# Optimization experiments

Measured on AMD Instinct MI355X. Metric: run time of the kernel, lower is better.

## Reference

```python
import jax, jax.numpy as jnp
import numpy as np

N_NODES = 50000
N_EDGES = 800000
IN_DIM = 256
HID = 64


def _gcn_conv(x, src, dst, W, b, num_nodes):
    # PyG GCNConv: h = D^{-1/2} (A + I) D^{-1/2} (x @ W) + b
    h = x @ W  # [N, out]
    loop = jnp.arange(num_nodes)
    s = jnp.concatenate([src, loop])  # add self-loops
    d = jnp.concatenate([dst, loop])
    deg = jax.ops.segment_sum(jnp.ones_like(s, dtype=h.dtype), d, num_segments=num_nodes)
    dinv = jnp.where(deg > 0, deg ** -0.5, 0.0)
    norm = dinv[s] * dinv[d]  # [E+N]
    msgs = h[s] * norm[:, None]  # gather + scale
    out = jax.ops.segment_sum(msgs, d, num_segments=num_nodes)  # scatter-add to dst
    return out + b


def setup_inputs() -> dict:
    key = jax.random.key(0)
    ks = jax.random.split(key, 8)
    x = jax.random.normal(ks[0], (N_NODES, IN_DIM), dtype=jnp.float32)
    edge_index = jax.random.randint(ks[1], (2, N_EDGES), 0, N_NODES, dtype=jnp.int64)
    # Glorot-ish init for weights
    W1 = jax.random.normal(ks[2], (IN_DIM, HID), dtype=jnp.float32) * (1.0 / np.sqrt(IN_DIM))
    b1 = jnp.zeros((HID,), dtype=jnp.float32)
    W2 = jax.random.normal(ks[3], (HID, HID), dtype=jnp.float32) * (1.0 / np.sqrt(HID))
    b2 = jnp.zeros((HID,), dtype=jnp.float32)
    Wc = jax.random.normal(ks[4], (HID, 1), dtype=jnp.float32) * (1.0 / np.sqrt(HID))
    bc = jnp.zeros((1,), dtype=jnp.float32)
    return {"x": x, "edge_index": edge_index, "W1": W1, "b1": b1, "W2": W2, "b2": b2, "Wc": Wc, "bc": bc}


def reference(x, edge_index, W1, b1, W2, b2, Wc, bc):
    num_nodes = x.shape[0]
    src, dst = edge_index[0], edge_index[1]
    h = jax.nn.relu(_gcn_conv(x, src, dst, W1, b1, num_nodes))
    h = jax.nn.relu(_gcn_conv(h, src, dst, W2, b2, num_nodes))
    return jax.nn.sigmoid(h @ Wc + bc)  # [N, 1]
```

## Files before the change

kernel.cpp:

```cpp
#include <hip/hip_runtime.h>
#include <math.h>

#define N_NODES 50000
#define N_EDGES 800000
#define IN_DIM 256
#define HID 64
#define BKT 256
#define NBKT ((N_NODES + BKT - 1) / BKT)
#define CAP 8192
#define CHUNK 4096
#define NCH ((N_EDGES + CHUNK - 1) / CHUNK)
#define NGB ((N_NODES + 63) / 64)

typedef short short8v __attribute__((ext_vector_type(8)));
typedef float f32x4 __attribute__((ext_vector_type(4)));
typedef unsigned uint4v __attribute__((ext_vector_type(4)));

__device__ __forceinline__ unsigned short f2bf(float f) {
  unsigned u = __builtin_bit_cast(unsigned, f);
  u += 0x7FFFu + ((u >> 16) & 1u);
  return (unsigned short)(u >> 16);
}
__device__ __forceinline__ unsigned pack2(float a, float b) {
  return (unsigned)f2bf(a) | ((unsigned)f2bf(b) << 16);
}
__device__ __forceinline__ float bfu_lo(unsigned u) {
  return __builtin_bit_cast(float, u << 16);
}
__device__ __forceinline__ float bfu_hi(unsigned u) {
  return __builtin_bit_cast(float, u & 0xFFFF0000u);
}

__global__ void k_prep(int* __restrict__ bcur, const float* __restrict__ W1,
                       const float* __restrict__ W2, unsigned short* __restrict__ Wt1,
                       unsigned short* __restrict__ Wt2) {
  const int t = threadIdx.x;
  if (blockIdx.x == 0) {
    bcur[t] = 0;
  } else if (blockIdx.x == 1) {
    for (int j = 0; j < 64; ++j) {
      int lin = j * 256 + t;
      int k = lin >> 6, c = lin & 63;
      Wt1[c * 256 + k] = f2bf(W1[lin]);
    }
  } else {
    for (int j = 0; j < 16; ++j) {
      int lin = j * 256 + t;
      int k = lin >> 6, c = lin & 63;
      Wt2[c * 64 + k] = f2bf(W2[lin]);
    }
  }
}

__global__ __launch_bounds__(256) void k_g1split(
    const float* __restrict__ X, const unsigned short* __restrict__ Wt1g,
    unsigned short* __restrict__ outA, const int* __restrict__ src,
    const int* __restrict__ dst, int* __restrict__ bcur, unsigned* __restrict__ ebuf) {
  __shared__ unsigned short Wl[64][IN_DIM + 8];
  __shared__ int cnt[NBKT];
  __shared__ int cur[NBKT];
  const int t = threadIdx.x;
  if (blockIdx.x < NGB) {
    const int lane = t & 63, wv = t >> 6;
#pragma unroll
    for (int j = 0; j < 8; ++j) {
      int grp = j * 256 + t;
      int r = grp >> 5, c = (grp & 31) * 8;
      *reinterpret_cast<short8v*>(&Wl[r][c]) =
          *reinterpret_cast<const short8v*>(&Wt1g[r * IN_DIM + c]);
    }
    const int row0 = blockIdx.x * 64;
    int r = row0 + wv * 16 + (lane & 15);
    if (r > N_NODES - 1) r = N_NODES - 1;
    const int kh = (lane >> 4) * 8;

    uint4v ap[8];
#pragma unroll
    for (int k0 = 0; k0 < 8; ++k0) {
      const float* Xp = X + (size_t)r * IN_DIM + k0 * 32 + kh;
      const float4 x0 = *reinterpret_cast<const float4*>(Xp);
      const float4 x1 = *reinterpret_cast<const float4*>(Xp + 4);
      uint4v p;
      p.x = pack2(x0.x, x0.y); p.y = pack2(x0.z, x0.w);
      p.z = pack2(x1.x, x1.y); p.w = pack2(x1.z, x1.w);
      ap[k0] = p;
    }
    __syncthreads();

    f32x4 acc[4] = {};
#pragma unroll
    for (int k0 = 0; k0 < 8; ++k0) {
      short8v a = __builtin_bit_cast(short8v, ap[k0]);
#pragma unroll
      for (int n = 0; n < 4; ++n) {
        short8v b = *reinterpret_cast<const short8v*>(&Wl[n * 16 + (lane & 15)][k0 * 32 + kh]);
        acc[n] = __builtin_amdgcn_mfma_f32_16x16x32_bf16(a, b, acc[n], 0, 0, 0);
      }
    }

    const int r0 = row0 + wv * 16;
#pragma unroll
    for (int j = 0; j < 4; ++j) {
      int rr = r0 + (lane >> 4) * 4 + j;
      if (rr < N_NODES) {
#pragma unroll
        for (int n = 0; n < 4; ++n)
          outA[(size_t)rr * 64 + n * 16 + (lane & 15)] = f2bf(acc[n][j]);
      }
    }
  } else {
    for (int i = t; i < NBKT; i += 256) cnt[i] = 0;
    __syncthreads();
    const int base = (blockIdx.x - NGB) * CHUNK;
#pragma unroll
    for (int i = 0; i < CHUNK / 256; ++i) {
      int e = base + i * 256 + t;
      if (e < N_EDGES) atomicAdd(&cnt[dst[e] >> 8], 1);
    }
    __syncthreads();
    for (int i = t; i < NBKT; i += 256) {
      int c = cnt[i];
      cur[i] = c ? (i * CAP + atomicAdd(&bcur[i], c)) : 0;
    }
    __syncthreads();
#pragma unroll
    for (int i = 0; i < CHUNK / 256; ++i) {
      int e = base + i * 256 + t;
      if (e < N_EDGES) {
        int d = dst[e];
        int p = atomicAdd(&cur[d >> 8], 1);
        ebuf[p] = ((unsigned)src[e] << 8) | (unsigned)(d & 255);
      }
    }
  }
}

__global__ void k_bucket(const unsigned* __restrict__ ebuf, const int* __restrict__ bcur,
                         int* __restrict__ rowptr, int* __restrict__ colidx,
                         float* __restrict__ dinv, unsigned short* __restrict__ hbuf) {
  __shared__ int sA[256];
  __shared__ int sB[256];
  __shared__ float sD[256];
  const int b = blockIdx.x, t = threadIdx.x;

  sA[t] = (t < NBKT) ? bcur[t] : 0;
  __syncthreads();
  for (int d = 1; d < 256; d <<= 1) {
    int v = sA[t];
    int a = (t >= d) ? sA[t - d] : 0;
    __syncthreads();
    sA[t] = v + a;
    __syncthreads();
  }
  const int prefix = (b == 0) ? 0 : sA[b - 1];
  const int cntb = bcur[b];
  const int sbeg = b * CAP, send = sbeg + cntb;
  __syncthreads();

  sA[t] = 0;
  __syncthreads();
  for (int i = sbeg + t; i < send; i += 256) atomicAdd(&sA[ebuf[i] & 255], 1);
  __syncthreads();
  const int myc = sA[t];
  sB[t] = myc;
  __syncthreads();
  for (int d = 1; d < 256; d <<= 1) {
    int v = sB[t];
    int a = (t >= d) ? sB[t - d] : 0;
    __syncthreads();
    sB[t] = v + a;
    __syncthreads();
  }
  const int node = b * BKT + t;
  const bool valid = node < N_NODES;
  const int ex = prefix + sB[t] - myc;
  const float dv = rsqrtf((float)(myc + 1));
  sD[t] = dv;
  if (valid) {
    rowptr[node] = ex;
    dinv[node] = dv;
    if (node == N_NODES - 1) rowptr[N_NODES] = N_EDGES;
  }
  __syncthreads();
  sB[t] = ex;
  __syncthreads();
  for (int i = sbeg + t; i < send; i += 256) {
    unsigned p = ebuf[i];
    int pos = atomicAdd(&sB[p & 255], 1);
    colidx[pos] = (int)(p >> 8);
  }

  const int rsub = t >> 3, f8 = (t & 7) * 8;
#pragma unroll
  for (int g = 0; g < 8; ++g) {
    int lr = g * 32 + rsub;
    int nd = b * BKT + lr;
    if (nd < N_NODES) {
      float s = sD[lr];
      unsigned short* hp = &hbuf[(size_t)nd * 64 + f8];
      uint4 hv = *reinterpret_cast<const uint4*>(hp);
      uint4 o;
      o.x = pack2(s * bfu_lo(hv.x), s * bfu_hi(hv.x));
      o.y = pack2(s * bfu_lo(hv.y), s * bfu_hi(hv.y));
      o.z = pack2(s * bfu_lo(hv.z), s * bfu_hi(hv.z));
      o.w = pack2(s * bfu_lo(hv.w), s * bfu_hi(hv.w));
      *reinterpret_cast<uint4*>(hp) = o;
    }
  }
}

#define EDGEP(hbuf, cc)                                                       \
  {                                                                           \
    uint4 w = *reinterpret_cast<const uint4*>(&hbuf[(size_t)(cc) * 64 + f0]); \
    acc0 += bfu_lo(w.x); acc1 += bfu_hi(w.x);                                 \
    acc2 += bfu_lo(w.y); acc3 += bfu_hi(w.y);                                 \
    acc4 += bfu_lo(w.z); acc5 += bfu_hi(w.z);                                 \
    acc6 += bfu_lo(w.w); acc7 += bfu_hi(w.w);                                 \
  }

#define GATHER_PLAIN(hbuf, EV, ENDV)                                               \
  uint4 sw = *reinterpret_cast<const uint4*>(&hbuf[(size_t)v * 64 + f0]);          \
  float acc0 = bfu_lo(sw.x), acc1 = bfu_hi(sw.x);                                  \
  float acc2 = bfu_lo(sw.y), acc3 = bfu_hi(sw.y);                                  \
  float acc4 = bfu_lo(sw.z), acc5 = bfu_hi(sw.z);                                  \
  float acc6 = bfu_lo(sw.w), acc7 = bfu_hi(sw.w);                                  \
  int e = EV;                                                                      \
  const int end = ENDV;                                                            \
  while (e < end && (e & 3)) { EDGEP(hbuf, col[e]); ++e; }                         \
  for (; e + 8 <= end; e += 8) {                                                   \
    int4 ca = *reinterpret_cast<const int4*>(&col[e]);                             \
    int4 cb = *reinterpret_cast<const int4*>(&col[e + 4]);                         \
    EDGEP(hbuf, ca.x); EDGEP(hbuf, ca.y); EDGEP(hbuf, ca.z); EDGEP(hbuf, ca.w);    \
    EDGEP(hbuf, cb.x); EDGEP(hbuf, cb.y); EDGEP(hbuf, cb.z); EDGEP(hbuf, cb.w);    \
  }                                                                                \
  for (; e + 4 <= end; e += 4) {                                                   \
    int4 cc = *reinterpret_cast<const int4*>(&col[e]);                             \
    EDGEP(hbuf, cc.x); EDGEP(hbuf, cc.y); EDGEP(hbuf, cc.z); EDGEP(hbuf, cc.w);    \
  }                                                                                \
  for (; e < end; ++e) { EDGEP(hbuf, col[e]); }

__global__ __launch_bounds__(256) void k_agg_gemm(
    const unsigned short* __restrict__ h, const int* __restrict__ rowptr,
    const int* __restrict__ col, const float* __restrict__ dinv,
    const float* __restrict__ bias, const unsigned short* __restrict__ Wt2g,
    unsigned short* __restrict__ out) {
  const int t = threadIdx.x, lane = t & 63, wv = t >> 6;
  const int g = lane >> 3, f0 = (lane & 7) * 8;
  const int vbase = blockIdx.x * 32;
  const int v = vbase + wv * 8 + g;
  const int lrow = wv * 8 + g;

  __shared__ unsigned short h1s[32][72];

  if (v < N_NODES) {
    const float sv = dinv[v];
    GATHER_PLAIN(h, rowptr[v], rowptr[v + 1])

    const float4 ba = *reinterpret_cast<const float4*>(&bias[f0]);
    const float4 bb = *reinterpret_cast<const float4*>(&bias[f0 + 4]);
    float v0 = fmaxf(fmaf(sv, acc0, ba.x), 0.0f);
    float v1 = fmaxf(fmaf(sv, acc1, ba.y), 0.0f);
    float v2 = fmaxf(fmaf(sv, acc2, ba.z), 0.0f);
    float v3 = fmaxf(fmaf(sv, acc3, ba.w), 0.0f);
    float v4 = fmaxf(fmaf(sv, acc4, bb.x), 0.0f);
    float v5 = fmaxf(fmaf(sv, acc5, bb.y), 0.0f);
    float v6 = fmaxf(fmaf(sv, acc6, bb.z), 0.0f);
    float v7 = fmaxf(fmaf(sv, acc7, bb.w), 0.0f);

    uint4 o;
    o.x = pack2(v0, v1); o.y = pack2(v2, v3);
    o.z = pack2(v4, v5); o.w = pack2(v6, v7);
    *reinterpret_cast<uint4*>(&h1s[lrow][f0]) = o;
  } else {
    uint4 z = {0, 0, 0, 0};
    *reinterpret_cast<uint4*>(&h1s[lrow][f0]) = z;
  }
  __syncthreads();

  const int kh = (lane >> 4) * 8;
  f32x4 acc2r[2] = {};
#pragma unroll
  for (int rt = 0; rt < 2; ++rt) {
#pragma unroll
    for (int k0 = 0; k0 < 64; k0 += 32) {
      short8v a = *reinterpret_cast<const short8v*>(&h1s[rt * 16 + (lane & 15)][k0 + kh]);
      short8v b = *reinterpret_cast<const short8v*>(
          Wt2g + (size_t)(wv * 16 + (lane & 15)) * 64 + k0 + kh);
      acc2r[rt] = __builtin_amdgcn_mfma_f32_16x16x32_bf16(a, b, acc2r[rt], 0, 0, 0);
    }
  }
#pragma unroll
  for (int rt = 0; rt < 2; ++rt) {
#pragma unroll
    for (int j = 0; j < 4; ++j) {
      int vg = vbase + rt * 16 + (lane >> 4) * 4 + j;
      if (vg < N_NODES)
        out[(size_t)vg * 64 + wv * 16 + (lane & 15)] = f2bf(acc2r[rt][j] * dinv[vg]);
    }
  }
}

__global__ __launch_bounds__(256) void k_agg_fin(
    const unsigned short* __restrict__ h, const int* __restrict__ rowptr,
    const int* __restrict__ col, const float* __restrict__ dinv,
    const float* __restrict__ bias, const float* __restrict__ Wc,
    const float* __restrict__ bc, float* __restrict__ out) {
  const int t = threadIdx.x, lane = t & 63;
  const int g = lane >> 3, f0 = (lane & 7) * 8;
  const int v = blockIdx.x * 32 + (t >> 6) * 8 + g;
  if (v >= N_NODES) return;

  GATHER_PLAIN(h, rowptr[v], rowptr[v + 1])

  const float sv = dinv[v];
  const float4 ba = *reinterpret_cast<const float4*>(&bias[f0]);
  const float4 bb = *reinterpret_cast<const float4*>(&bias[f0 + 4]);
  const float4 wa = *reinterpret_cast<const float4*>(&Wc[f0]);
  const float4 wb = *reinterpret_cast<const float4*>(&Wc[f0 + 4]);
  float p = fmaxf(fmaf(sv, acc0, ba.x), 0.0f) * wa.x +
            fmaxf(fmaf(sv, acc1, ba.y), 0.0f) * wa.y +
            fmaxf(fmaf(sv, acc2, ba.z), 0.0f) * wa.z +
            fmaxf(fmaf(sv, acc3, ba.w), 0.0f) * wa.w +
            fmaxf(fmaf(sv, acc4, bb.x), 0.0f) * wb.x +
            fmaxf(fmaf(sv, acc5, bb.y), 0.0f) * wb.y +
            fmaxf(fmaf(sv, acc6, bb.z), 0.0f) * wb.z +
            fmaxf(fmaf(sv, acc7, bb.w), 0.0f) * wb.w;
  p += __shfl_xor(p, 1);
  p += __shfl_xor(p, 2);
  p += __shfl_xor(p, 4);
  if ((lane & 7) == 0) out[v] = 1.0f / (1.0f + expf(-(p + bc[0])));
}

extern "C" void kernel_launch(void* const* d_in, const int* in_sizes, int n_in,
                              void* d_out, int out_size, void* d_ws, size_t ws_size,
                              hipStream_t stream) {
  const float* x  = (const float*)d_in[0];
  const int*   ei = (const int*)d_in[1];
  const float* W1 = (const float*)d_in[2];
  const float* b1 = (const float*)d_in[3];
  const float* W2 = (const float*)d_in[4];
  const float* b2 = (const float*)d_in[5];
  const float* Wc = (const float*)d_in[6];
  const float* bc = (const float*)d_in[7];
  float* out = (float*)d_out;

  const int* src = ei;
  const int* dst = ei + N_EDGES;

  unsigned* w = (unsigned*)d_ws;
  int*   bcur   = (int*)(w + 0);
  int*   rowptr = (int*)(w + 256);
  int*   colidx = (int*)(w + 50688);
  unsigned* ebuf = w + 850688;
  float* dinv   = (float*)(w + 2456320);
  unsigned short* Wt1g = (unsigned short*)(w + 2506496);
  unsigned short* Wt2g = (unsigned short*)(w + 2514688);
  unsigned short* A_bf = (unsigned short*)(w + 2516736);
  unsigned short* B_bf = (unsigned short*)(w + 4116736);

  k_prep<<<3, 256, 0, stream>>>(bcur, W1, W2, Wt1g, Wt2g);
  k_g1split<<<NGB + NCH, 256, 0, stream>>>(x, Wt1g, A_bf, src, dst, bcur, ebuf);
  k_bucket<<<NBKT, 256, 0, stream>>>(ebuf, bcur, rowptr, colidx, dinv, A_bf);

  const int NAB = (N_NODES + 31) / 32;
  k_agg_gemm<<<NAB, 256, 0, stream>>>(A_bf, rowptr, colidx, dinv, b1, Wt2g, B_bf);
  k_agg_fin<<<NAB, 256, 0, stream>>>(B_bf, rowptr, colidx, dinv, b2, Wc, bc, out);
}
```

Baseline: 100.7 us.

## Split edge aggregation into feature-half passes and separate layer-2 GEMM kernel

Each aggregation now runs as two passes, each gathering only half of the 64 features (64 bytes per neighbor row), with 4 lanes per node instead of 8. Halving the gathered working set per pass is meant to improve cache hit rates for the random neighbor gathers. The fused aggregate+GEMM kernel is split into a standalone MFMA GEMM kernel, and the final classifier dot product is accumulated across the two passes through a partial buffer. In exchange it adds kernel launches, extra global round-trips of the intermediate features, and reads the CSR indices twice.

```diff
diff --git a/kernel.cpp b/kernel.cpp
--- a/kernel.cpp
+++ b/kernel.cpp
@@ -209,126 +209,137 @@
   }
 }
 
-#define EDGEP(hbuf, cc)                                                       \
-  {                                                                           \
-    uint4 w = *reinterpret_cast<const uint4*>(&hbuf[(size_t)(cc) * 64 + f0]); \
-    acc0 += bfu_lo(w.x); acc1 += bfu_hi(w.x);                                 \
-    acc2 += bfu_lo(w.y); acc3 += bfu_hi(w.y);                                 \
-    acc4 += bfu_lo(w.z); acc5 += bfu_hi(w.z);                                 \
-    acc6 += bfu_lo(w.w); acc7 += bfu_hi(w.w);                                 \
-  }
-
-#define GATHER_PLAIN(hbuf, EV, ENDV)                                               \
-  uint4 sw = *reinterpret_cast<const uint4*>(&hbuf[(size_t)v * 64 + f0]);          \
-  float acc0 = bfu_lo(sw.x), acc1 = bfu_hi(sw.x);                                  \
-  float acc2 = bfu_lo(sw.y), acc3 = bfu_hi(sw.y);                                  \
-  float acc4 = bfu_lo(sw.z), acc5 = bfu_hi(sw.z);                                  \
-  float acc6 = bfu_lo(sw.w), acc7 = bfu_hi(sw.w);                                  \
-  int e = EV;                                                                      \
-  const int end = ENDV;                                                            \
-  while (e < end && (e & 3)) { EDGEP(hbuf, col[e]); ++e; }                         \
+#define EHALF(hbuf, cc)                                                          \
+  {                                                                              \
+    uint4 w = *reinterpret_cast<const uint4*>(&hbuf[(size_t)(cc) * 64 + foff]);  \
+    a0 += bfu_lo(w.x); a1 += bfu_hi(w.x);                                        \
+    a2 += bfu_lo(w.y); a3 += bfu_hi(w.y);                                        \
+    a4 += bfu_lo(w.z); a5 += bfu_hi(w.z);                                        \
+    a6 += bfu_lo(w.w); a7 += bfu_hi(w.w);                                        \
+  }
+
+#define GATHER_HALF(hbuf)                                                          \
+  int e = rowptr[v];                                                               \
+  const int end = rowptr[v + 1];                                                   \
+  uint4 sw = *reinterpret_cast<const uint4*>(&hbuf[(size_t)v * 64 + foff]);        \
+  float a0 = bfu_lo(sw.x), a1 = bfu_hi(sw.x);                                      \
+  float a2 = bfu_lo(sw.y), a3 = bfu_hi(sw.y);                                      \
+  float a4 = bfu_lo(sw.z), a5 = bfu_hi(sw.z);                                      \
+  float a6 = bfu_lo(sw.w), a7 = bfu_hi(sw.w);                                      \
+  while (e < end && (e & 3)) { EHALF(hbuf, col[e]); ++e; }                         \
   for (; e + 8 <= end; e += 8) {                                                   \
     int4 ca = *reinterpret_cast<const int4*>(&col[e]);                             \
     int4 cb = *reinterpret_cast<const int4*>(&col[e + 4]);                         \
-    EDGEP(hbuf, ca.x); EDGEP(hbuf, ca.y); EDGEP(hbuf, ca.z); EDGEP(hbuf, ca.w);    \
-    EDGEP(hbuf, cb.x); EDGEP(hbuf, cb.y); EDGEP(hbuf, cb.z); EDGEP(hbuf, cb.w);    \
+    EHALF(hbuf, ca.x); EHALF(hbuf, ca.y); EHALF(hbuf, ca.z); EHALF(hbuf, ca.w);    \
+    EHALF(hbuf, cb.x); EHALF(hbuf, cb.y); EHALF(hbuf, cb.z); EHALF(hbuf, cb.w);    \
   }                                                                                \
   for (; e + 4 <= end; e += 4) {                                                   \
     int4 cc = *reinterpret_cast<const int4*>(&col[e]);                             \
-    EDGEP(hbuf, cc.x); EDGEP(hbuf, cc.y); EDGEP(hbuf, cc.z); EDGEP(hbuf, cc.w);    \
+    EHALF(hbuf, cc.x); EHALF(hbuf, cc.y); EHALF(hbuf, cc.z); EHALF(hbuf, cc.w);    \
   }                                                                                \
-  for (; e < end; ++e) { EDGEP(hbuf, col[e]); }
-
-__global__ __launch_bounds__(256) void k_agg_gemm(
+  for (; e < end; ++e) { EHALF(hbuf, col[e]); }
+
+template <int HALF>
+__global__ __launch_bounds__(256) void k_agg1h(
     const unsigned short* __restrict__ h, const int* __restrict__ rowptr,
     const int* __restrict__ col, const float* __restrict__ dinv,
-    const float* __restrict__ bias, const unsigned short* __restrict__ Wt2g,
-    unsigned short* __restrict__ out) {
+    const float* __restrict__ bias, unsigned short* __restrict__ h1) {
+  const int t = threadIdx.x, lane = t & 63;
+  const int grp = lane >> 2, foff = HALF * 32 + (lane & 3) * 8;
+  const int v = blockIdx.x * 64 + (t >> 6) * 16 + grp;
+  if (v >= N_NODES) return;
+
+  GATHER_HALF(h)
+
+  const float sv = dinv[v];
+  const float4 ba = *reinterpret_cast<const float4*>(&bias[foff]);
+  const float4 bb = *reinterpret_cast<const float4*>(&bias[foff + 4]);
+  float v0 = fmaxf(fmaf(sv, a0, ba.x), 0.0f);
+  float v1 = fmaxf(fmaf(sv, a1, ba.y), 0.0f);
+  float v2 = fmaxf(fmaf(sv, a2, ba.z), 0.0f);
+  float v3 = fmaxf(fmaf(sv, a3, ba.w), 0.0f);
+  float v4 = fmaxf(fmaf(sv, a4, bb.x), 0.0f);
+  float v5 = fmaxf(fmaf(sv, a5, bb.y), 0.0f);
+  float v6 = fmaxf(fmaf(sv, a6, bb.z), 0.0f);
+  float v7 = fmaxf(fmaf(sv, a7, bb.w), 0.0f);
+
+  uint4 o;
+  o.x = pack2(v0, v1); o.y = pack2(v2, v3);
+  o.z = pack2(v4, v5); o.w = pack2(v6, v7);
+  *reinterpret_cast<uint4*>(&h1[(size_t)v * 64 + foff]) = o;
+}
+
+__global__ __launch_bounds__(256) void k_gemm2(const unsigned short* __restrict__ h1,
+                                               const unsigned short* __restrict__ Wt2g,
+                                               const float* __restrict__ dinv,
+                                               unsigned short* __restrict__ out) {
   const int t = threadIdx.x, lane = t & 63, wv = t >> 6;
-  const int g = lane >> 3, f0 = (lane & 7) * 8;
-  const int vbase = blockIdx.x * 32;
-  const int v = vbase + wv * 8 + g;
-  const int lrow = wv * 8 + g;
-
-  __shared__ unsigned short h1s[32][72];
-
-  if (v < N_NODES) {
-    const float sv = dinv[v];
-    GATHER_PLAIN(h, rowptr[v], rowptr[v + 1])
-
-    const float4 ba = *reinterpret_cast<const float4*>(&bias[f0]);
-    const float4 bb = *reinterpret_cast<const float4*>(&bias[f0 + 4]);
-    float v0 = fmaxf(fmaf(sv, acc0, ba.x), 0.0f);
-    float v1 = fmaxf(fmaf(sv, acc1, ba.y), 0.0f);
-    float v2 = fmaxf(fmaf(sv, acc2, ba.z), 0.0f);
-    float v3 = fmaxf(fmaf(sv, acc3, ba.w), 0.0f);
-    float v4 = fmaxf(fmaf(sv, acc4, bb.x), 0.0f);
-    float v5 = fmaxf(fmaf(sv, acc5, bb.y), 0.0f);
-    float v6 = fmaxf(fmaf(sv, acc6, bb.z), 0.0f);
-    float v7 = fmaxf(fmaf(sv, acc7, bb.w), 0.0f);
-
-    uint4 o;
-    o.x = pack2(v0, v1); o.y = pack2(v2, v3);
-    o.z = pack2(v4, v5); o.w = pack2(v6, v7);
-    *reinterpret_cast<uint4*>(&h1s[lrow][f0]) = o;
-  } else {
-    uint4 z = {0, 0, 0, 0};
-    *reinterpret_cast<uint4*>(&h1s[lrow][f0]) = z;
-  }
-  __syncthreads();
-
+  const int row0 = blockIdx.x * 64;
+  int r = row0 + wv * 16 + (lane & 15);
+  if (r > N_NODES - 1) r = N_NODES - 1;
   const int kh = (lane >> 4) * 8;
-  f32x4 acc2r[2] = {};
-#pragma unroll
-  for (int rt = 0; rt < 2; ++rt) {
-#pragma unroll
-    for (int k0 = 0; k0 < 64; k0 += 32) {
-      short8v a = *reinterpret_cast<const short8v*>(&h1s[rt * 16 + (lane & 15)][k0 + kh]);
+
+  f32x4 acc[4] = {};
+#pragma unroll
+  for (int k0 = 0; k0 < 64; k0 += 32) {
+    short8v a = *reinterpret_cast<const short8v*>(&h1[(size_t)r * 64 + k0 + kh]);
+#pragma unroll
+    for (int n = 0; n < 4; ++n) {
       short8v b = *reinterpret_cast<const short8v*>(
-          Wt2g + (size_t)(wv * 16 + (lane & 15)) * 64 + k0 + kh);
-      acc2r[rt] = __builtin_amdgcn_mfma_f32_16x16x32_bf16(a, b, acc2r[rt], 0, 0, 0);
-    }
-  }
-#pragma unroll
-  for (int rt = 0; rt < 2; ++rt) {
-#pragma unroll
-    for (int j = 0; j < 4; ++j) {
-      int vg = vbase + rt * 16 + (lane >> 4) * 4 + j;
-      if (vg < N_NODES)
-        out[(size_t)vg * 64 + wv * 16 + (lane & 15)] = f2bf(acc2r[rt][j] * dinv[vg]);
-    }
-  }
-}
-
-__global__ __launch_bounds__(256) void k_agg_fin(
+          Wt2g + (size_t)(n * 16 + (lane & 15)) * 64 + k0 + kh);
+      acc[n] = __builtin_amdgcn_mfma_f32_16x16x32_bf16(a, b, acc[n], 0, 0, 0);
+    }
+  }
+
+  const int r0 = row0 + wv * 16;
+#pragma unroll
+  for (int j = 0; j < 4; ++j) {
+    int rr = r0 + (lane >> 4) * 4 + j;
+    if (rr < N_NODES) {
+      float s = dinv[rr];
+#pragma unroll
+      for (int n = 0; n < 4; ++n)
+        out[(size_t)rr * 64 + n * 16 + (lane & 15)] = f2bf(acc[n][j] * s);
+    }
+  }
+}
+
+template <int HALF>
+__global__ __launch_bounds__(256) void k_agg2(
     const unsigned short* __restrict__ h, const int* __restrict__ rowptr,
     const int* __restrict__ col, const float* __restrict__ dinv,
     const float* __restrict__ bias, const float* __restrict__ Wc,
-    const float* __restrict__ bc, float* __restrict__ out) {
+    const float* __restrict__ bc, float* __restrict__ pacc,
+    float* __restrict__ out) {
   const int t = threadIdx.x, lane = t & 63;
-  const int g = lane >> 3, f0 = (lane & 7) * 8;
-  const int v = blockIdx.x * 32 + (t >> 6) * 8 + g;
+  const int grp = lane >> 2, foff = HALF * 32 + (lane & 3) * 8;
+  const int v = blockIdx.x * 64 + (t >> 6) * 16 + grp;
   if (v >= N_NODES) return;
 
-  GATHER_PLAIN(h, rowptr[v], rowptr[v + 1])
+  GATHER_HALF(h)
 
   const float sv = dinv[v];
-  const float4 ba = *reinterpret_cast<const float4*>(&bias[f0]);
-  const float4 bb = *reinterpret_cast<const float4*>(&bias[f0 + 4]);
-  const float4 wa = *reinterpret_cast<const float4*>(&Wc[f0]);
-  const float4 wb = *reinterpret_cast<const float4*>(&Wc[f0 + 4]);
-  float p = fmaxf(fmaf(sv, acc0, ba.x), 0.0f) * wa.x +
-            fmaxf(fmaf(sv, acc1, ba.y), 0.0f) * wa.y +
-            fmaxf(fmaf(sv, acc2, ba.z), 0.0f) * wa.z +
-            fmaxf(fmaf(sv, acc3, ba.w), 0.0f) * wa.w +
-            fmaxf(fmaf(sv, acc4, bb.x), 0.0f) * wb.x +
-            fmaxf(fmaf(sv, acc5, bb.y), 0.0f) * wb.y +
-            fmaxf(fmaf(sv, acc6, bb.z), 0.0f) * wb.z +
-            fmaxf(fmaf(sv, acc7, bb.w), 0.0f) * wb.w;
+  const float4 ba = *reinterpret_cast<const float4*>(&bias[foff]);
+  const float4 bb = *reinterpret_cast<const float4*>(&bias[foff + 4]);
+  const float4 wa = *reinterpret_cast<const float4*>(&Wc[foff]);
+  const float4 wb = *reinterpret_cast<const float4*>(&Wc[foff + 4]);
+  float p = fmaxf(fmaf(sv, a0, ba.x), 0.0f) * wa.x +
+            fmaxf(fmaf(sv, a1, ba.y), 0.0f) * wa.y +
+            fmaxf(fmaf(sv, a2, ba.z), 0.0f) * wa.z +
+            fmaxf(fmaf(sv, a3, ba.w), 0.0f) * wa.w +
+            fmaxf(fmaf(sv, a4, bb.x), 0.0f) * wb.x +
+            fmaxf(fmaf(sv, a5, bb.y), 0.0f) * wb.y +
+            fmaxf(fmaf(sv, a6, bb.z), 0.0f) * wb.z +
+            fmaxf(fmaf(sv, a7, bb.w), 0.0f) * wb.w;
   p += __shfl_xor(p, 1);
   p += __shfl_xor(p, 2);
-  p += __shfl_xor(p, 4);
-  if ((lane & 7) == 0) out[v] = 1.0f / (1.0f + expf(-(p + bc[0])));
+  if ((lane & 3) == 0) {
+    if (HALF == 0) {
+      pacc[v] = p;
+    } else {
+      out[v] = 1.0f / (1.0f + expf(-(p + pacc[v] + bc[0])));
+    }
+  }
 }
 
 extern "C" void kernel_launch(void* const* d_in, const int* in_sizes, int n_in,
@@ -353,16 +364,20 @@
   int*   colidx = (int*)(w + 50688);
   unsigned* ebuf = w + 850688;
   float* dinv   = (float*)(w + 2456320);
-  unsigned short* Wt1g = (unsigned short*)(w + 2506496);
-  unsigned short* Wt2g = (unsigned short*)(w + 2514688);
-  unsigned short* A_bf = (unsigned short*)(w + 2516736);
-  unsigned short* B_bf = (unsigned short*)(w + 4116736);
+  float* pacc   = (float*)(w + 2506496);
+  unsigned short* Wt1g = (unsigned short*)(w + 2556672);
+  unsigned short* Wt2g = (unsigned short*)(w + 2564864);
+  unsigned short* A_bf = (unsigned short*)(w + 2566912);
+  unsigned short* B_bf = (unsigned short*)(w + 4166912);
 
   k_prep<<<3, 256, 0, stream>>>(bcur, W1, W2, Wt1g, Wt2g);
   k_g1split<<<NGB + NCH, 256, 0, stream>>>(x, Wt1g, A_bf, src, dst, bcur, ebuf);
   k_bucket<<<NBKT, 256, 0, stream>>>(ebuf, bcur, rowptr, colidx, dinv, A_bf);
 
-  const int NAB = (N_NODES + 31) / 32;
-  k_agg_gemm<<<NAB, 256, 0, stream>>>(A_bf, rowptr, colidx, dinv, b1, Wt2g, B_bf);
-  k_agg_fin<<<NAB, 256, 0, stream>>>(B_bf, rowptr, colidx, dinv, b2, Wc, bc, out);
-}
+  const int NHB = (N_NODES + 63) / 64;
+  k_agg1h<0><<<NHB, 256, 0, stream>>>(A_bf, rowptr, colidx, dinv, b1, B_bf);
+  k_agg1h<1><<<NHB, 256, 0, stream>>>(A_bf, rowptr, colidx, dinv, b1, B_bf);
+  k_gemm2<<<NHB, 256, 0, stream>>>(B_bf, Wt2g, dinv, A_bf);
+  k_agg2<0><<<NHB, 256, 0, stream>>>(A_bf, rowptr, colidx, dinv, b2, Wc, bc, pacc, out);
+  k_agg2<1><<<NHB, 256, 0, stream>>>(A_bf, rowptr, colidx, dinv, b2, Wc, bc, pacc, out);
+}
```

Result: slower. 125.9 us (+25.1%).
